# Optimization experiments

Measured on AMD Instinct MI355X. Metric: run time of the kernel, lower is better.

## Reference

```python
import jax, jax.numpy as jnp
import numpy as np

N_NODES = 100000
N_REL = 500
N_EDGES = 600000
DIM = 128


def setup_inputs() -> dict:
    key = jax.random.key(0)
    ks = jax.random.split(key, 10)
    ent = jax.random.normal(ks[0], (N_NODES, DIM), dtype=jnp.float32)
    rel = jax.random.normal(ks[1], (N_REL, DIM), dtype=jnp.float32)
    edge_index = jax.random.randint(ks[2], (2, N_EDGES), 0, N_NODES, dtype=jnp.int64)
    edge_type = jax.random.randint(ks[3], (N_EDGES,), 0, N_REL, dtype=jnp.int64)
    s = 1.0 / np.sqrt(DIM)
    W_self = jax.random.uniform(ks[4], (DIM, DIM), jnp.float32, -s, s)
    b_self = jax.random.uniform(ks[5], (DIM,), jnp.float32, -s, s)
    W_nei = jax.random.uniform(ks[6], (DIM, DIM), jnp.float32, -s, s)
    b_nei = jax.random.uniform(ks[7], (DIM,), jnp.float32, -s, s)
    W_rel = jax.random.uniform(ks[8], (DIM, DIM), jnp.float32, -s, s)
    b_rel = jax.random.uniform(ks[9], (DIM,), jnp.float32, -s, s)
    return {
        "ent": ent, "rel": rel, "edge_index": edge_index, "edge_type": edge_type,
        "W_self": W_self, "b_self": b_self,
        "W_nei": W_nei, "b_nei": b_nei,
        "W_rel": W_rel, "b_rel": b_rel,
    }


def reference(ent, rel, edge_index, edge_type, W_self, b_self, W_nei, b_nei, W_rel, b_rel):
    src, dst = edge_index[0], edge_index[1]
    # gather -> sigmoid-gate -> scatter-add
    msg = ent[src] * jax.nn.sigmoid(rel[edge_type])          # [E, dim]
    agg = jax.ops.segment_sum(msg, dst, num_segments=ent.shape[0])  # [N, dim]
    out_ent = jax.nn.relu(ent @ W_self.T + b_self + agg @ W_nei.T + b_nei)
    out_rel = rel @ W_rel.T + b_rel
    return (out_ent, out_rel)
```

## Files before the change

kernel.cpp:

```cpp
#include <hip/hip_runtime.h>
#include <hip/hip_bf16.h>
#include <math.h>

#define DIM 128

typedef __bf16 bf8 __attribute__((ext_vector_type(8)));
typedef float f4 __attribute__((ext_vector_type(4)));

struct __align__(8) bf16x4 { __hip_bfloat162 a, b; };

__global__ __launch_bounds__(256) void prep_kernel(
    const float* __restrict__ rel,
    const float* __restrict__ Ws,
    const float* __restrict__ Wn,
    const float* __restrict__ Wr,
    __hip_bfloat16* __restrict__ sigb,
    __hip_bfloat16* __restrict__ Wcat,
    float* __restrict__ Wt_rel,
    int nSig, int sigBlocks) {
    int b = blockIdx.x;
    if (b < sigBlocks) {
        int i = b * 256 + threadIdx.x;
        if (i < nSig) {
            float x = rel[i];
            sigb[i] = __float2bfloat16(1.0f / (1.0f + expf(-x)));
        }
    } else if (b < sigBlocks + 32) {
        int idx = (b - sigBlocks) * 256 + threadIdx.x;
        int j  = idx >> 6;
        int k0 = (idx & 63) * 4;
        const float* src = (k0 < DIM) ? &Ws[j * DIM + k0] : &Wn[j * DIM + (k0 - DIM)];
        float4 v = *(const float4*)src;
        bf16x4 o;
        o.a.x = __float2bfloat16(v.x);
        o.a.y = __float2bfloat16(v.y);
        o.b.x = __float2bfloat16(v.z);
        o.b.y = __float2bfloat16(v.w);
        *(bf16x4*)&Wcat[(size_t)j * 256 + k0] = o;
    } else {
        int id = (b - sigBlocks - 32) * 256 + threadIdx.x;
        int k = id >> 7;
        int j = id & 127;
        Wt_rel[id] = Wr[j * DIM + k];
    }
}

__global__ __launch_bounds__(256) void conv_hist_kernel(
    const float* __restrict__ ent,
    __hip_bfloat16* __restrict__ xcat,
    const int* __restrict__ edge_index,
    int* __restrict__ counts,
    int N, int E, int convBlocks) {
    if ((int)blockIdx.x < convBlocks) {
        long long tid = (long long)blockIdx.x * 256 + threadIdx.x;
        int row = (int)(tid >> 5);
        int q   = (int)(tid & 31);
        if (row >= N) return;
        float4 v = *(const float4*)&ent[(size_t)row * DIM + q * 4];
        bf16x4 o;
        o.a.x = __float2bfloat16(v.x);
        o.a.y = __float2bfloat16(v.y);
        o.b.x = __float2bfloat16(v.z);
        o.b.y = __float2bfloat16(v.w);
        *(bf16x4*)&xcat[(size_t)row * 256 + q * 4] = o;
    } else {
        int e = (blockIdx.x - convBlocks) * 256 + threadIdx.x;
        if (e < E) atomicAdd(&counts[edge_index[E + e]], 1);
    }
}

#define SCAN_TPB 256
#define SCAN_IPT 4
#define SCAN_IPB 1024

__global__ void scan_pass1(int* __restrict__ data,
                           int* __restrict__ blockSums, int N) {
    __shared__ int ts[SCAN_TPB];
    int t = threadIdx.x;
    int base = blockIdx.x * SCAN_IPB + t * SCAN_IPT;
    int v[SCAN_IPT];
    int s = 0;
    #pragma unroll
    for (int i = 0; i < SCAN_IPT; ++i) {
        int idx = base + i;
        v[i] = (idx < N) ? data[idx] : 0;
        s += v[i];
    }
    ts[t] = s;
    __syncthreads();
    for (int off = 1; off < SCAN_TPB; off <<= 1) {
        int x = (t >= off) ? ts[t - off] : 0;
        __syncthreads();
        ts[t] += x;
        __syncthreads();
    }
    int excl = ts[t] - s;
    #pragma unroll
    for (int i = 0; i < SCAN_IPT; ++i) {
        int idx = base + i;
        if (idx < N) data[idx] = excl;
        excl += v[i];
    }
    if (t == SCAN_TPB - 1) blockSums[blockIdx.x] = ts[t];
}

__global__ void scan_pass2(int* __restrict__ blockSums, int nb) {
    __shared__ int s[128];
    int t = threadIdx.x;
    int v = (t < nb) ? blockSums[t] : 0;
    s[t] = v;
    __syncthreads();
    for (int off = 1; off < 128; off <<= 1) {
        int x = (t >= off) ? s[t - off] : 0;
        __syncthreads();
        s[t] += x;
        __syncthreads();
    }
    if (t < nb) blockSums[t] = s[t] - v;
}

__global__ void scan_pass3(int* __restrict__ offs, const int* __restrict__ blockSums,
                           int* __restrict__ cursor, int N, int E) {
    int i = blockIdx.x * blockDim.x + threadIdx.x;
    if (i < N) {
        int o = offs[i] + blockSums[i >> 10];
        offs[i] = o;
        cursor[i] = o;
    }
    if (i == 0) offs[N] = E;
}

__global__ void scatter_ids_kernel(const int* __restrict__ edge_index,
                                   const int* __restrict__ edge_type,
                                   int* __restrict__ cursor,
                                   unsigned* __restrict__ spack, int E) {
    int e = blockIdx.x * blockDim.x + threadIdx.x;
    if (e >= E) return;
    int dst = edge_index[E + e];
    int p = atomicAdd(&cursor[dst], 1);
    spack[p] = (unsigned)edge_index[e] | ((unsigned)edge_type[e] << 17);
}

__global__ __launch_bounds__(256) void aggregate_kernel(
    const __hip_bfloat16* __restrict__ xcat,
    const __hip_bfloat16* __restrict__ sigb,
    const int* __restrict__ offs,
    const unsigned* __restrict__ spack,
    __hip_bfloat16* __restrict__ xcat_w, int N) {
    int wid  = (int)((blockIdx.x * (long long)blockDim.x + threadIdx.x) >> 6);
    int lane = threadIdx.x & 63;
    if (wid >= N) return;
    int beg = offs[wid], end = offs[wid + 1];
    float ax0 = 0.f, ay0 = 0.f, ax1 = 0.f, ay1 = 0.f;
    int e = beg;
    for (; e + 4 <= end; e += 4) {
        unsigned p0 = spack[e + 0];
        unsigned p1 = spack[e + 1];
        unsigned p2 = spack[e + 2];
        unsigned p3 = spack[e + 3];
        __hip_bfloat162 v0 = *(const __hip_bfloat162*)&xcat[(size_t)(p0 & 0x1FFFFu) * 256 + lane * 2];
        __hip_bfloat162 v1 = *(const __hip_bfloat162*)&xcat[(size_t)(p1 & 0x1FFFFu) * 256 + lane * 2];
        __hip_bfloat162 v2 = *(const __hip_bfloat162*)&xcat[(size_t)(p2 & 0x1FFFFu) * 256 + lane * 2];
        __hip_bfloat162 v3 = *(const __hip_bfloat162*)&xcat[(size_t)(p3 & 0x1FFFFu) * 256 + lane * 2];
        __hip_bfloat162 g0 = *(const __hip_bfloat162*)&sigb[(size_t)(p0 >> 17) * DIM + lane * 2];
        __hip_bfloat162 g1 = *(const __hip_bfloat162*)&sigb[(size_t)(p1 >> 17) * DIM + lane * 2];
        __hip_bfloat162 g2 = *(const __hip_bfloat162*)&sigb[(size_t)(p2 >> 17) * DIM + lane * 2];
        __hip_bfloat162 g3 = *(const __hip_bfloat162*)&sigb[(size_t)(p3 >> 17) * DIM + lane * 2];
        ax0 += __bfloat162float(v0.x) * __bfloat162float(g0.x);
        ay0 += __bfloat162float(v0.y) * __bfloat162float(g0.y);
        ax1 += __bfloat162float(v1.x) * __bfloat162float(g1.x);
        ay1 += __bfloat162float(v1.y) * __bfloat162float(g1.y);
        ax0 += __bfloat162float(v2.x) * __bfloat162float(g2.x);
        ay0 += __bfloat162float(v2.y) * __bfloat162float(g2.y);
        ax1 += __bfloat162float(v3.x) * __bfloat162float(g3.x);
        ay1 += __bfloat162float(v3.y) * __bfloat162float(g3.y);
    }
    for (; e < end; ++e) {
        unsigned p = spack[e];
        __hip_bfloat162 v = *(const __hip_bfloat162*)&xcat[(size_t)(p & 0x1FFFFu) * 256 + lane * 2];
        __hip_bfloat162 g = *(const __hip_bfloat162*)&sigb[(size_t)(p >> 17) * DIM + lane * 2];
        ax0 += __bfloat162float(v.x) * __bfloat162float(g.x);
        ay0 += __bfloat162float(v.y) * __bfloat162float(g.y);
    }
    __hip_bfloat162 o;
    o.x = __float2bfloat16(ax0 + ax1);
    o.y = __float2bfloat16(ay0 + ay1);
    *(__hip_bfloat162*)&xcat_w[(size_t)wid * 256 + 128 + lane * 2] = o;
}

__global__ __launch_bounds__(128) void relout_kernel(
    const float* __restrict__ rel,
    const float* __restrict__ Wt_rel,
    const float* __restrict__ b_rel,
    float* __restrict__ out_rel) {
    __shared__ float rrow[DIM];
    int b = blockIdx.x;
    int t = threadIdx.x;
    rrow[t] = rel[(size_t)b * DIM + t];
    __syncthreads();
    float acc = b_rel[t];
    #pragma unroll 8
    for (int k = 0; k < DIM; ++k) {
        acc += rrow[k] * Wt_rel[k * DIM + t];
    }
    out_rel[(size_t)b * DIM + t] = acc;
}

__global__ __launch_bounds__(256) void gemm_mfma_kernel(
    const __hip_bfloat16* __restrict__ xcat,
    const __hip_bfloat16* __restrict__ Wcat,
    const float* __restrict__ b_self,
    const float* __restrict__ b_nei,
    float* __restrict__ out, int N) {
    __shared__ __hip_bfloat16 Bs[128][264];

    int t    = threadIdx.x;
    int wave = t >> 6;
    int lane = t & 63;
    int quad = lane >> 4;
    int r16  = lane & 15;

    {
        int r = t >> 1, h = t & 1;
        const float4* src = (const float4*)&Wcat[(size_t)r * 256 + h * 128];
        #pragma unroll
        for (int i = 0; i < 16; ++i) {
            *(float4*)&Bs[r][h * 128 + i * 8] = src[i];
        }
    }
    __syncthreads();

    int row0 = blockIdx.x * 128 + wave * 32;

    bf8 a[2][8];
    #pragma unroll
    for (int rt = 0; rt < 2; ++rt) {
        int m = row0 + rt * 16 + r16;
        if (m > N - 1) m = N - 1;
        const __hip_bfloat16* ap = &xcat[(size_t)m * 256 + quad * 8];
        #pragma unroll
        for (int ks = 0; ks < 8; ++ks) {
            a[rt][ks] = *(const bf8*)(ap + ks * 32);
        }
    }

    f4 acc[2][8];
    #pragma unroll
    for (int rt = 0; rt < 2; ++rt)
        #pragma unroll
        for (int ct = 0; ct < 8; ++ct)
            acc[rt][ct] = (f4){0.f, 0.f, 0.f, 0.f};

    #pragma unroll
    for (int ks = 0; ks < 8; ++ks) {
        #pragma unroll
        for (int ct = 0; ct < 8; ++ct) {
            bf8 b = *(const bf8*)&Bs[ct * 16 + r16][ks * 32 + quad * 8];
            acc[0][ct] = __builtin_amdgcn_mfma_f32_16x16x32_bf16(a[0][ks], b, acc[0][ct], 0, 0, 0);
            acc[1][ct] = __builtin_amdgcn_mfma_f32_16x16x32_bf16(a[1][ks], b, acc[1][ct], 0, 0, 0);
        }
    }

    float bias[8];
    #pragma unroll
    for (int ct = 0; ct < 8; ++ct) {
        int col = ct * 16 + r16;
        bias[ct] = b_self[col] + b_nei[col];
    }
    #pragma unroll
    for (int rt = 0; rt < 2; ++rt) {
        #pragma unroll
        for (int i = 0; i < 4; ++i) {
            int m = row0 + rt * 16 + quad * 4 + i;
            if (m < N) {
                #pragma unroll
                for (int ct = 0; ct < 8; ++ct) {
                    float v = acc[rt][ct][i] + bias[ct];
                    out[(size_t)m * DIM + ct * 16 + r16] = fmaxf(v, 0.f);
                }
            }
        }
    }
}

extern "C" void kernel_launch(void* const* d_in, const int* in_sizes, int n_in,
                              void* d_out, int out_size, void* d_ws, size_t ws_size,
                              hipStream_t stream) {
    const float* ent        = (const float*)d_in[0];
    const float* rel        = (const float*)d_in[1];
    const int*   edge_index = (const int*)d_in[2];
    const int*   edge_type  = (const int*)d_in[3];
    const float* W_self     = (const float*)d_in[4];
    const float* b_self     = (const float*)d_in[5];
    const float* W_nei      = (const float*)d_in[6];
    const float* b_nei      = (const float*)d_in[7];
    const float* W_rel      = (const float*)d_in[8];
    const float* b_rel      = (const float*)d_in[9];

    const int N = in_sizes[0] / DIM;
    const int R = in_sizes[1] / DIM;
    const int E = in_sizes[3];

    float* out     = (float*)d_out;
    float* out_rel = out + (size_t)N * DIM;
    __hip_bfloat16* xcat = (__hip_bfloat16*)d_out;

    __hip_bfloat16* sigb = (__hip_bfloat16*)d_ws;
    float* Wt_rel  = (float*)(sigb + (size_t)R * DIM);
    __hip_bfloat16* Wcat = (__hip_bfloat16*)(Wt_rel + DIM * DIM);
    int*   offs    = (int*)(Wcat + 128 * 256);
    int*   cursor  = offs + (N + 8);
    int*   bsums   = cursor + (N + 8);
    unsigned* spack = (unsigned*)(bsums + 128);

    const int scanBlocks = (N + SCAN_IPB - 1) / SCAN_IPB;
    const int nSig = R * DIM;
    const int sigBlocks = (nSig + 255) / 256;

    prep_kernel<<<sigBlocks + 32 + 64, 256, 0, stream>>>(
        rel, W_self, W_nei, W_rel, sigb, Wcat, Wt_rel, nSig, sigBlocks);

    hipMemsetAsync(offs, 0, (size_t)(N + 1) * sizeof(int), stream);
    {
        int convBlocks = (int)(((long long)N * 32 + 255) / 256);
        int histBlocks = (E + 255) / 256;
        conv_hist_kernel<<<convBlocks + histBlocks, 256, 0, stream>>>(
            ent, xcat, edge_index, offs, N, E, convBlocks);
    }

    scan_pass1<<<scanBlocks, SCAN_TPB, 0, stream>>>(offs, bsums, N);
    scan_pass2<<<1, 128, 0, stream>>>(bsums, scanBlocks);
    scan_pass3<<<(N + 255) / 256, 256, 0, stream>>>(offs, bsums, cursor, N, E);
    scatter_ids_kernel<<<(E + 255) / 256, 256, 0, stream>>>(
        edge_index, edge_type, cursor, spack, E);

    {
        long long threads = (long long)N * 64;
        aggregate_kernel<<<(int)((threads + 255) / 256), 256, 0, stream>>>(
            xcat, sigb, offs, spack, xcat, N);
    }

    relout_kernel<<<R, DIM, 0, stream>>>(rel, Wt_rel, b_rel, out_rel);

    {
        int blocks = (N + 127) / 128;
        gemm_mfma_kernel<<<blocks, 256, 0, stream>>>(xcat, Wcat, b_self, b_nei, out, N);
    }
}
```

Measured before the change: 250.3 us.

## Fold memset into prep, single-block scan, masked aggregate tail, vectorized GEMM epilogue

Zeroing of the offsets array moves into the prep kernel, replacing a separate memset. The three-pass scan becomes one 1024-thread single-block kernel in which each thread walks a contiguous chunk of about 98 elements. The aggregate loop drops its scalar tail and instead runs masked 4-wide iterations. The GEMM swaps its MFMA operands so each lane holds four consecutive output columns, allowing float4 bias loads and float4 stores. These changes cut launch count and store transactions, but the single-block scan walks strided chunks serially and leaves the rest of the GPU idle, and the masked tail issues redundant loads.

```diff
diff --git a/kernel.cpp b/kernel.cpp
--- a/kernel.cpp
+++ b/kernel.cpp
@@ -17,7 +17,8 @@
     __hip_bfloat16* __restrict__ sigb,
     __hip_bfloat16* __restrict__ Wcat,
     float* __restrict__ Wt_rel,
-    int nSig, int sigBlocks) {
+    int* __restrict__ offs,
+    int nSig, int sigBlocks, int N) {
     int b = blockIdx.x;
     if (b < sigBlocks) {
         int i = b * 256 + threadIdx.x;
@@ -37,11 +38,14 @@
         o.b.x = __float2bfloat16(v.z);
         o.b.y = __float2bfloat16(v.w);
         *(bf16x4*)&Wcat[(size_t)j * 256 + k0] = o;
-    } else {
+    } else if (b < sigBlocks + 32 + 64) {
         int id = (b - sigBlocks - 32) * 256 + threadIdx.x;
         int k = id >> 7;
         int j = id & 127;
         Wt_rel[id] = Wr[j * DIM + k];
+    } else {
+        int i = (b - sigBlocks - 32 - 64) * 256 + threadIdx.x;
+        if (i <= N) offs[i] = 0;
     }
 }
 
@@ -69,65 +73,32 @@
     }
 }
 
-#define SCAN_TPB 256
-#define SCAN_IPT 4
-#define SCAN_IPB 1024
-
-__global__ void scan_pass1(int* __restrict__ data,
-                           int* __restrict__ blockSums, int N) {
-    __shared__ int ts[SCAN_TPB];
+#define SCB_T 1024
+__global__ __launch_bounds__(1024) void scan_all_kernel(
+    int* __restrict__ offs, int* __restrict__ cursor, int N, int E) {
+    __shared__ int ts[SCB_T];
     int t = threadIdx.x;
-    int base = blockIdx.x * SCAN_IPB + t * SCAN_IPT;
-    int v[SCAN_IPT];
+    const int C = (N + SCB_T - 1) / SCB_T;
+    int lo = t * C;
+    int hi = lo + C; if (hi > N) hi = N; if (lo > N) lo = N;
     int s = 0;
-    #pragma unroll
-    for (int i = 0; i < SCAN_IPT; ++i) {
-        int idx = base + i;
-        v[i] = (idx < N) ? data[idx] : 0;
-        s += v[i];
-    }
+    for (int i = lo; i < hi; ++i) s += offs[i];
     ts[t] = s;
     __syncthreads();
-    for (int off = 1; off < SCAN_TPB; off <<= 1) {
+    for (int off = 1; off < SCB_T; off <<= 1) {
         int x = (t >= off) ? ts[t - off] : 0;
         __syncthreads();
         ts[t] += x;
         __syncthreads();
     }
-    int excl = ts[t] - s;
-    #pragma unroll
-    for (int i = 0; i < SCAN_IPT; ++i) {
-        int idx = base + i;
-        if (idx < N) data[idx] = excl;
-        excl += v[i];
-    }
-    if (t == SCAN_TPB - 1) blockSums[blockIdx.x] = ts[t];
-}
-
-__global__ void scan_pass2(int* __restrict__ blockSums, int nb) {
-    __shared__ int s[128];
-    int t = threadIdx.x;
-    int v = (t < nb) ? blockSums[t] : 0;
-    s[t] = v;
-    __syncthreads();
-    for (int off = 1; off < 128; off <<= 1) {
-        int x = (t >= off) ? s[t - off] : 0;
-        __syncthreads();
-        s[t] += x;
-        __syncthreads();
-    }
-    if (t < nb) blockSums[t] = s[t] - v;
-}
-
-__global__ void scan_pass3(int* __restrict__ offs, const int* __restrict__ blockSums,
-                           int* __restrict__ cursor, int N, int E) {
-    int i = blockIdx.x * blockDim.x + threadIdx.x;
-    if (i < N) {
-        int o = offs[i] + blockSums[i >> 10];
-        offs[i] = o;
-        cursor[i] = o;
-    }
-    if (i == 0) offs[N] = E;
+    int run = ts[t] - s;
+    for (int i = lo; i < hi; ++i) {
+        int v = offs[i];
+        offs[i] = run;
+        cursor[i] = run;
+        run += v;
+    }
+    if (t == 0) offs[N] = E;
 }
 
 __global__ void scatter_ids_kernel(const int* __restrict__ edge_index,
@@ -152,12 +123,12 @@
     if (wid >= N) return;
     int beg = offs[wid], end = offs[wid + 1];
     float ax0 = 0.f, ay0 = 0.f, ax1 = 0.f, ay1 = 0.f;
-    int e = beg;
-    for (; e + 4 <= end; e += 4) {
-        unsigned p0 = spack[e + 0];
-        unsigned p1 = spack[e + 1];
-        unsigned p2 = spack[e + 2];
-        unsigned p3 = spack[e + 3];
+    for (int e = beg; e < end; e += 4) {
+        int r = end - e;
+        unsigned p0 = spack[e];
+        unsigned p1 = spack[r > 1 ? e + 1 : e];
+        unsigned p2 = spack[r > 2 ? e + 2 : e];
+        unsigned p3 = spack[r > 3 ? e + 3 : e];
         __hip_bfloat162 v0 = *(const __hip_bfloat162*)&xcat[(size_t)(p0 & 0x1FFFFu) * 256 + lane * 2];
         __hip_bfloat162 v1 = *(const __hip_bfloat162*)&xcat[(size_t)(p1 & 0x1FFFFu) * 256 + lane * 2];
         __hip_bfloat162 v2 = *(const __hip_bfloat162*)&xcat[(size_t)(p2 & 0x1FFFFu) * 256 + lane * 2];
@@ -166,21 +137,17 @@
         __hip_bfloat162 g1 = *(const __hip_bfloat162*)&sigb[(size_t)(p1 >> 17) * DIM + lane * 2];
         __hip_bfloat162 g2 = *(const __hip_bfloat162*)&sigb[(size_t)(p2 >> 17) * DIM + lane * 2];
         __hip_bfloat162 g3 = *(const __hip_bfloat162*)&sigb[(size_t)(p3 >> 17) * DIM + lane * 2];
+        float m1 = (r > 1) ? 1.f : 0.f;
+        float m2 = (r > 2) ? 1.f : 0.f;
+        float m3 = (r > 3) ? 1.f : 0.f;
         ax0 += __bfloat162float(v0.x) * __bfloat162float(g0.x);
         ay0 += __bfloat162float(v0.y) * __bfloat162float(g0.y);
-        ax1 += __bfloat162float(v1.x) * __bfloat162float(g1.x);
-        ay1 += __bfloat162float(v1.y) * __bfloat162float(g1.y);
-        ax0 += __bfloat162float(v2.x) * __bfloat162float(g2.x);
-        ay0 += __bfloat162float(v2.y) * __bfloat162float(g2.y);
-        ax1 += __bfloat162float(v3.x) * __bfloat162float(g3.x);
-        ay1 += __bfloat162float(v3.y) * __bfloat162float(g3.y);
-    }
-    for (; e < end; ++e) {
-        unsigned p = spack[e];
-        __hip_bfloat162 v = *(const __hip_bfloat162*)&xcat[(size_t)(p & 0x1FFFFu) * 256 + lane * 2];
-        __hip_bfloat162 g = *(const __hip_bfloat162*)&sigb[(size_t)(p >> 17) * DIM + lane * 2];
-        ax0 += __bfloat162float(v.x) * __bfloat162float(g.x);
-        ay0 += __bfloat162float(v.y) * __bfloat162float(g.y);
+        ax1 += m1 * (__bfloat162float(v1.x) * __bfloat162float(g1.x));
+        ay1 += m1 * (__bfloat162float(v1.y) * __bfloat162float(g1.y));
+        ax0 += m2 * (__bfloat162float(v2.x) * __bfloat162float(g2.x));
+        ay0 += m2 * (__bfloat162float(v2.y) * __bfloat162float(g2.y));
+        ax1 += m3 * (__bfloat162float(v3.x) * __bfloat162float(g3.x));
+        ay1 += m3 * (__bfloat162float(v3.y) * __bfloat162float(g3.y));
     }
     __hip_bfloat162 o;
     o.x = __float2bfloat16(ax0 + ax1);
@@ -207,11 +174,11 @@
 }
 
 __global__ __launch_bounds__(256) void gemm_mfma_kernel(
-    const __hip_bfloat16* __restrict__ xcat,
+    const __hip_bfloat16* xcat,
     const __hip_bfloat16* __restrict__ Wcat,
     const float* __restrict__ b_self,
     const float* __restrict__ b_nei,
-    float* __restrict__ out, int N) {
+    float* out, int N) {
     __shared__ __hip_bfloat16 Bs[128][264];
 
     int t    = threadIdx.x;
@@ -232,52 +199,56 @@
 
     int row0 = blockIdx.x * 128 + wave * 32;
 
-    bf8 a[2][8];
-    #pragma unroll
-    for (int rt = 0; rt < 2; ++rt) {
-        int m = row0 + rt * 16 + r16;
+    bf8 x[2][8];
+    #pragma unroll
+    for (int mt = 0; mt < 2; ++mt) {
+        int m = row0 + mt * 16 + r16;
         if (m > N - 1) m = N - 1;
-        const __hip_bfloat16* ap = &xcat[(size_t)m * 256 + quad * 8];
+        const __hip_bfloat16* xp = &xcat[(size_t)m * 256 + quad * 8];
         #pragma unroll
         for (int ks = 0; ks < 8; ++ks) {
-            a[rt][ks] = *(const bf8*)(ap + ks * 32);
+            x[mt][ks] = *(const bf8*)(xp + ks * 32);
         }
     }
 
     f4 acc[2][8];
     #pragma unroll
-    for (int rt = 0; rt < 2; ++rt)
+    for (int mt = 0; mt < 2; ++mt)
         #pragma unroll
-        for (int ct = 0; ct < 8; ++ct)
-            acc[rt][ct] = (f4){0.f, 0.f, 0.f, 0.f};
+        for (int jt = 0; jt < 8; ++jt)
+            acc[mt][jt] = (f4){0.f, 0.f, 0.f, 0.f};
 
     #pragma unroll
     for (int ks = 0; ks < 8; ++ks) {
         #pragma unroll
-        for (int ct = 0; ct < 8; ++ct) {
-            bf8 b = *(const bf8*)&Bs[ct * 16 + r16][ks * 32 + quad * 8];
-            acc[0][ct] = __builtin_amdgcn_mfma_f32_16x16x32_bf16(a[0][ks], b, acc[0][ct], 0, 0, 0);
-            acc[1][ct] = __builtin_amdgcn_mfma_f32_16x16x32_bf16(a[1][ks], b, acc[1][ct], 0, 0, 0);
-        }
-    }
-
-    float bias[8];
-    #pragma unroll
-    for (int ct = 0; ct < 8; ++ct) {
-        int col = ct * 16 + r16;
-        bias[ct] = b_self[col] + b_nei[col];
-    }
-    #pragma unroll
-    for (int rt = 0; rt < 2; ++rt) {
-        #pragma unroll
-        for (int i = 0; i < 4; ++i) {
-            int m = row0 + rt * 16 + quad * 4 + i;
-            if (m < N) {
-                #pragma unroll
-                for (int ct = 0; ct < 8; ++ct) {
-                    float v = acc[rt][ct][i] + bias[ct];
-                    out[(size_t)m * DIM + ct * 16 + r16] = fmaxf(v, 0.f);
-                }
+        for (int jt = 0; jt < 8; ++jt) {
+            bf8 w = *(const bf8*)&Bs[jt * 16 + r16][ks * 32 + quad * 8];
+            acc[0][jt] = __builtin_amdgcn_mfma_f32_16x16x32_bf16(w, x[0][ks], acc[0][jt], 0, 0, 0);
+            acc[1][jt] = __builtin_amdgcn_mfma_f32_16x16x32_bf16(w, x[1][ks], acc[1][jt], 0, 0, 0);
+        }
+    }
+
+    f4 bias4[8];
+    #pragma unroll
+    for (int jt = 0; jt < 8; ++jt) {
+        const float4 bs = *(const float4*)&b_self[jt * 16 + quad * 4];
+        const float4 bn = *(const float4*)&b_nei[jt * 16 + quad * 4];
+        bias4[jt] = (f4){bs.x + bn.x, bs.y + bn.y, bs.z + bn.z, bs.w + bn.w};
+    }
+
+    #pragma unroll
+    for (int mt = 0; mt < 2; ++mt) {
+        int m = row0 + mt * 16 + r16;
+        if (m < N) {
+            #pragma unroll
+            for (int jt = 0; jt < 8; ++jt) {
+                f4 v = acc[mt][jt] + bias4[jt];
+                float4 o;
+                o.x = fmaxf(v[0], 0.f);
+                o.y = fmaxf(v[1], 0.f);
+                o.z = fmaxf(v[2], 0.f);
+                o.w = fmaxf(v[3], 0.f);
+                *(float4*)&out[(size_t)m * DIM + jt * 16 + quad * 4] = o;
             }
         }
     }
@@ -310,17 +281,15 @@
     __hip_bfloat16* Wcat = (__hip_bfloat16*)(Wt_rel + DIM * DIM);
     int*   offs    = (int*)(Wcat + 128 * 256);
     int*   cursor  = offs + (N + 8);
-    int*   bsums   = cursor + (N + 8);
-    unsigned* spack = (unsigned*)(bsums + 128);
-
-    const int scanBlocks = (N + SCAN_IPB - 1) / SCAN_IPB;
+    unsigned* spack = (unsigned*)(cursor + (N + 8));
+
     const int nSig = R * DIM;
     const int sigBlocks = (nSig + 255) / 256;
-
-    prep_kernel<<<sigBlocks + 32 + 64, 256, 0, stream>>>(
-        rel, W_self, W_nei, W_rel, sigb, Wcat, Wt_rel, nSig, sigBlocks);
-
-    hipMemsetAsync(offs, 0, (size_t)(N + 1) * sizeof(int), stream);
+    const int zeroBlocks = (N + 1 + 255) / 256;
+
+    prep_kernel<<<sigBlocks + 32 + 64 + zeroBlocks, 256, 0, stream>>>(
+        rel, W_self, W_nei, W_rel, sigb, Wcat, Wt_rel, offs, nSig, sigBlocks, N);
+
     {
         int convBlocks = (int)(((long long)N * 32 + 255) / 256);
         int histBlocks = (E + 255) / 256;
@@ -328,9 +297,8 @@
             ent, xcat, edge_index, offs, N, E, convBlocks);
     }
 
-    scan_pass1<<<scanBlocks, SCAN_TPB, 0, stream>>>(offs, bsums, N);
-    scan_pass2<<<1, 128, 0, stream>>>(bsums, scanBlocks);
-    scan_pass3<<<(N + 255) / 256, 256, 0, stream>>>(offs, bsums, cursor, N, E);
+    scan_all_kernel<<<1, SCB_T, 0, stream>>>(offs, cursor, N, E);
+
     scatter_ids_kernel<<<(E + 255) / 256, 256, 0, stream>>>(
         edge_index, edge_type, cursor, spack, E);
 
```

Measured after the change: 461.6 us. 84.4% more time.
